# Kernel optimization log

Hardware: AMD Instinct MI355X
Metric: run time of the kernel (lower is better)

## Reference

```python
import jax, jax.numpy as jnp
import numpy as np

NUM_PATCHES = 128  # K centers from farthest point sampling
PATCH_SIZE = 32    # neighbors per patch (KNN)


def setup_inputs() -> dict:
    key = jax.random.key(0)
    points = jax.random.normal(key, (32, 8192, 3), dtype=jnp.float32)
    return {"points": points}


def _fps(points, K):
    """Farthest point sampling. points: [B, N, 3] -> idx [B, K] (int32).
    Deterministic start at index 0 (original uses random_start_point=True;
    only the start index differs)."""
    B, N, _ = points.shape
    start = jnp.zeros((B,), dtype=jnp.int32)

    def step(carry, _):
        mind, last = carry  # mind: [B, N] running min sq-dist, last: [B]
        last_pt = jnp.take_along_axis(points, last[:, None, None], axis=1)[:, 0]  # [B, 3]
        d = jnp.sum((points - last_pt[:, None, :]) ** 2, axis=-1)  # [B, N]
        mind = jnp.minimum(mind, d)
        nxt = jnp.argmax(mind, axis=1).astype(jnp.int32)
        return (mind, nxt), last

    init = (jnp.full((B, N), jnp.inf, dtype=points.dtype), start)
    _, idxs = jax.lax.scan(step, init, None, length=K)  # [K, B]
    return jnp.transpose(idxs)  # [B, K]


def reference(points):
    # FPS center selection
    fps_idx = _fps(points, NUM_PATCHES)  # [B, K]
    centers = jnp.take_along_axis(points, fps_idx[:, :, None], axis=1)  # [B, K, 3]
    # Brute-force KNN: squared distances centers->points, [B, K, N]
    d2 = (jnp.sum(centers * centers, axis=-1)[:, :, None]
          + jnp.sum(points * points, axis=-1)[:, None, :]
          - 2.0 * jnp.einsum('bkd,bnd->bkn', centers, points))
    # k smallest distances, sorted ascending (top_k of negated d2 is descending)
    _, idx = jax.lax.top_k(-d2, PATCH_SIZE)  # [B, K, patch_size]
    return idx, centers
```

## Files before the change

kernel.cpp:

```cpp
#include <hip/hip_runtime.h>

#define BB 32
#define NN 8192
#define KK 128
#define PP 32
#define IDX_COUNT (BB * KK * PP)
#define XCHG_WORDS (BB * KK * 3)
#define XCHG_BYTES (XCHG_WORDS * 4)

#define DPP_RED_U64(v, CMP)                                                   \
    {                                                                         \
        _Pragma("unroll")                                                     \
        for (int s = 0; s < 6; ++s) {                                         \
            const int ctrl = (s == 0) ? 0x111 : (s == 1) ? 0x112 :            \
                             (s == 2) ? 0x114 : (s == 3) ? 0x118 :            \
                             (s == 4) ? 0x142 : 0x143;                        \
            unsigned lo = (unsigned)v, hi = (unsigned)(v >> 32);              \
            unsigned slo, shi;                                                \
            switch (ctrl) {                                                   \
            case 0x111:                                                       \
                slo = (unsigned)__builtin_amdgcn_update_dpp((int)lo, (int)lo, 0x111, 0xf, 0xf, false); \
                shi = (unsigned)__builtin_amdgcn_update_dpp((int)hi, (int)hi, 0x111, 0xf, 0xf, false); break; \
            case 0x112:                                                       \
                slo = (unsigned)__builtin_amdgcn_update_dpp((int)lo, (int)lo, 0x112, 0xf, 0xf, false); \
                shi = (unsigned)__builtin_amdgcn_update_dpp((int)hi, (int)hi, 0x112, 0xf, 0xf, false); break; \
            case 0x114:                                                       \
                slo = (unsigned)__builtin_amdgcn_update_dpp((int)lo, (int)lo, 0x114, 0xf, 0xf, false); \
                shi = (unsigned)__builtin_amdgcn_update_dpp((int)hi, (int)hi, 0x114, 0xf, 0xf, false); break; \
            case 0x118:                                                       \
                slo = (unsigned)__builtin_amdgcn_update_dpp((int)lo, (int)lo, 0x118, 0xf, 0xf, false); \
                shi = (unsigned)__builtin_amdgcn_update_dpp((int)hi, (int)hi, 0x118, 0xf, 0xf, false); break; \
            case 0x142:                                                       \
                slo = (unsigned)__builtin_amdgcn_update_dpp((int)lo, (int)lo, 0x142, 0xf, 0xf, false); \
                shi = (unsigned)__builtin_amdgcn_update_dpp((int)hi, (int)hi, 0x142, 0xf, 0xf, false); break; \
            default:                                                          \
                slo = (unsigned)__builtin_amdgcn_update_dpp((int)lo, (int)lo, 0x143, 0xf, 0xf, false); \
                shi = (unsigned)__builtin_amdgcn_update_dpp((int)hi, (int)hi, 0x143, 0xf, 0xf, false); break; \
            }                                                                 \
            const unsigned long long sv = ((unsigned long long)shi << 32) | slo; \
            if (sv CMP v) v = sv;                                             \
        }                                                                     \
    }

__device__ __forceinline__ unsigned long long readlane63_u64(unsigned long long v) {
    const unsigned lo = (unsigned)__builtin_amdgcn_readlane((int)(unsigned)v, 63);
    const unsigned hi = (unsigned)__builtin_amdgcn_readlane((int)(unsigned)(v >> 32), 63);
    return ((unsigned long long)hi << 32) | lo;
}

__device__ __forceinline__ void publish_word(unsigned* p, float v) {
    __hip_atomic_store(p, __float_as_uint(v), __ATOMIC_RELAXED,
                       __HIP_MEMORY_SCOPE_AGENT);
}
__device__ __forceinline__ float poll_word(const unsigned* p) {
    unsigned u = __hip_atomic_load(p, __ATOMIC_RELAXED, __HIP_MEMORY_SCOPE_AGENT);
    while (u == 0xFFFFFFFFu) {
        __builtin_amdgcn_s_sleep(8);
        u = __hip_atomic_load(p, __ATOMIC_RELAXED, __HIP_MEMORY_SCOPE_AGENT);
    }
    return __uint_as_float(u);
}

#define BAR_LDS() asm volatile("s_waitcnt lgkmcnt(0)\n\ts_barrier" ::: "memory")

#define CACHE_INS(kk, m1, m2, m3, m4)                                   \
    {                                                                   \
        const bool c1 = (kk) < m1, c2 = (kk) < m2,                      \
                   c3 = (kk) < m3, c4 = (kk) < m4;                      \
        m4 = c3 ? m3 : (c4 ? (kk) : m4);                                \
        m3 = c2 ? m2 : (c3 ? (kk) : m3);                                \
        m2 = c1 ? m1 : (c2 ? (kk) : m2);                                \
        m1 = c1 ? (kk) : m1;                                            \
    }

__global__ __launch_bounds__(1024) void clear_kernel(unsigned* __restrict__ xchg) {
    const int i = blockIdx.x * 1024 + threadIdx.x;
    xchg[i] = 0xFFFFFFFFu;
}

__global__ __launch_bounds__(512) void fused_kernel(
    const float* __restrict__ pts, float* __restrict__ out,
    unsigned* __restrict__ xchg)
{
#pragma clang fp contract(off)
    __shared__ __align__(16) unsigned char smem_raw[131072];
    const int t = threadIdx.x;
    const int lane = t & 63, wid = t >> 6;

    if (blockIdx.x < BB) {
        const int b = blockIdx.x;
        const float* p = pts + (size_t)b * NN * 3;
        float* pts3 = (float*)smem_raw;
        float* cbuf = (float*)(smem_raw + 98304);
        unsigned long long* wkf =
            (unsigned long long*)(smem_raw + 98304 + 1536);

        if (t == 0) {
            unsigned* dst = xchg + (unsigned)b * KK * 3u;
            publish_word(dst + 0, p[0]);
            publish_word(dst + 1, p[1]);
            publish_word(dst + 2, p[2]);
        }

        float px[16], py[16], pz[16], mind[16];
#pragma unroll
        for (int i = 0; i < 16; ++i) {
            const int idx = t + i * 512;
            const float x = p[idx * 3 + 0], y = p[idx * 3 + 1], z = p[idx * 3 + 2];
            px[i] = x; py[i] = y; pz[i] = z; mind[i] = __builtin_inff();
            pts3[idx * 3 + 0] = x; pts3[idx * 3 + 1] = y; pts3[idx * 3 + 2] = z;
        }
        __syncthreads();

        float lx = pts3[0], ly = pts3[1], lz = pts3[2];
        if (t == 0) { cbuf[0] = lx; cbuf[1] = ly; cbuf[2] = lz; }

        for (int k = 0; k < KK - 1; ++k) {
            float best = -1.0f; unsigned bidx = 0;
#pragma unroll
            for (int i = 0; i < 16; ++i) {
                const float dx = px[i] - lx, dy = py[i] - ly, dz = pz[i] - lz;
                const float d = (dx * dx + dy * dy) + dz * dz;
                const float m = mind[i] < d ? mind[i] : d;
                mind[i] = m;
                if (m > best) { best = m; bidx = (unsigned)(t + i * 512); }
            }
            union { float f; unsigned u; } cv; cv.f = best;
            unsigned long long key = ((unsigned long long)cv.u << 32)
                                   | (0xFFFFFFFFu - bidx);
            DPP_RED_U64(key, >);
            if (lane == 63) wkf[(k & 1) * 8 + wid] = key;
            BAR_LDS();
            unsigned long long w = wkf[(k & 1) * 8];
#pragma unroll
            for (int i = 1; i < 8; ++i) {
                const unsigned long long o = wkf[(k & 1) * 8 + i];
                if (o > w) w = o;
            }
            const unsigned last = 0xFFFFFFFFu - (unsigned)(w & 0xFFFFFFFFu);
            lx = pts3[last * 3 + 0];
            ly = pts3[last * 3 + 1];
            lz = pts3[last * 3 + 2];
            if (t == 0) {
                cbuf[(k + 1) * 3 + 0] = lx;
                cbuf[(k + 1) * 3 + 1] = ly;
                cbuf[(k + 1) * 3 + 2] = lz;
                unsigned* dst = xchg + ((unsigned)b * KK + (unsigned)(k + 1)) * 3u;
                publish_word(dst + 0, lx);
                publish_word(dst + 1, ly);
                publish_word(dst + 2, lz);
            }
        }
        __syncthreads();
        if (t < KK * 3)
            out[IDX_COUNT + b * (KK * 3) + t] = cbuf[t];
    } else {
        const int blk = blockIdx.x - BB;
        const int b = blk >> 2, kblk = blk & 3;
        float4* sp = (float4*)smem_raw;
        const float* p = pts + (size_t)b * NN * 3;
#pragma unroll
        for (int i = 0; i < 16; ++i) {
            const int idx = t + i * 512;
            const float x = p[idx * 3 + 0], y = p[idx * 3 + 1], z = p[idx * 3 + 2];
            sp[idx] = make_float4(x, y, z, (x * x + y * y) + z * z);
        }
        __syncthreads();

        for (int u = 0; u < 4; ++u) {
            const int c = kblk + 4 * wid + 32 * u;
            const unsigned* src = xchg + ((unsigned)b * KK + (unsigned)c) * 3u;
            const float cx = poll_word(src + 0);
            const float cy = poll_word(src + 1);
            const float cz = poll_word(src + 2);
            const float cc = (cx * cx + cy * cy) + cz * cz;

            unsigned long long m1 = ~0ull, m2 = ~0ull, m3 = ~0ull, m4 = ~0ull;
#pragma unroll 4
            for (int i = 0; i < 128; ++i) {
                const int idx = lane + i * 64;
                const float4 q = sp[idx];
                const float dot = (cx * q.x + cy * q.y) + cz * q.z;
                float d2 = (cc + q.w) - (2.0f * dot);
                d2 = d2 + 0.0f;
                union { float f; unsigned u; } cv; cv.f = d2;
                unsigned uu = cv.u;
                uu = (uu & 0x80000000u) ? ~uu : (uu | 0x80000000u);
                const unsigned long long kk2 =
                    ((unsigned long long)uu << 32) | (unsigned)idx;
                CACHE_INS(kk2, m1, m2, m3, m4);
            }

            float resv = 0.0f;
            for (int j = 0; j < PP; ++j) {
                unsigned long long r = m1;
                DPP_RED_U64(r, <);
                const unsigned long long best = readlane63_u64(r);
                if (lane == j) resv = (float)(unsigned)(best & 0xFFFFFFFFu);
                if (m1 == best) { m1 = m2; m2 = m3; m3 = m4; m4 = ~0ull; }
                if (m1 == ~0ull) {
                    for (int i = 0; i < 128; ++i) {
                        const int idx = lane + i * 64;
                        const float4 q = sp[idx];
                        const float dot = (cx * q.x + cy * q.y) + cz * q.z;
                        float d2 = (cc + q.w) - (2.0f * dot);
                        d2 = d2 + 0.0f;
                        union { float f; unsigned u; } cv; cv.f = d2;
                        unsigned uu = cv.u;
                        uu = (uu & 0x80000000u) ? ~uu : (uu | 0x80000000u);
                        const unsigned long long kk2 =
                            ((unsigned long long)uu << 32) | (unsigned)idx;
                        if (kk2 > best) CACHE_INS(kk2, m1, m2, m3, m4);
                    }
                }
            }
            if (lane < PP)
                out[(size_t)(b * KK + c) * PP + lane] = resv;
        }
    }
}

__global__ __launch_bounds__(512) void fps_kernel(
    const float* __restrict__ pts, float* __restrict__ out)
{
#pragma clang fp contract(off)
    const int b = blockIdx.x;
    const int t = threadIdx.x;
    const float* p = pts + (size_t)b * NN * 3;

    __shared__ float pts3[NN * 3];
    __shared__ float cbuf[KK * 3];
    __shared__ unsigned long long wk[2][8];

    float px[16], py[16], pz[16], mind[16];
#pragma unroll
    for (int i = 0; i < 16; ++i) {
        const int idx = t + i * 512;
        const float x = p[idx * 3 + 0], y = p[idx * 3 + 1], z = p[idx * 3 + 2];
        px[i] = x; py[i] = y; pz[i] = z; mind[i] = __builtin_inff();
        pts3[idx * 3 + 0] = x; pts3[idx * 3 + 1] = y; pts3[idx * 3 + 2] = z;
    }
    __syncthreads();

    float lx = pts3[0], ly = pts3[1], lz = pts3[2];
    if (t == 0) { cbuf[0] = lx; cbuf[1] = ly; cbuf[2] = lz; }
    const int lane = t & 63, wid = t >> 6;

    for (int k = 0; k < KK - 1; ++k) {
        float best = -1.0f; unsigned bidx = 0;
#pragma unroll
        for (int i = 0; i < 16; ++i) {
            const float dx = px[i] - lx, dy = py[i] - ly, dz = pz[i] - lz;
            const float d = (dx * dx + dy * dy) + dz * dz;
            const float m = mind[i] < d ? mind[i] : d;
            mind[i] = m;
            if (m > best) { best = m; bidx = (unsigned)(t + i * 512); }
        }
        union { float f; unsigned u; } cv; cv.f = best;
        unsigned long long key = ((unsigned long long)cv.u << 32)
                               | (0xFFFFFFFFu - bidx);
        DPP_RED_U64(key, >);
        if (lane == 63) wk[k & 1][wid] = key;
        __syncthreads();
        unsigned long long w = wk[k & 1][0];
#pragma unroll
        for (int i = 1; i < 8; ++i) {
            const unsigned long long o = wk[k & 1][i];
            if (o > w) w = o;
        }
        const unsigned last = 0xFFFFFFFFu - (unsigned)(w & 0xFFFFFFFFu);
        lx = pts3[last * 3 + 0];
        ly = pts3[last * 3 + 1];
        lz = pts3[last * 3 + 2];
        if (t == 0) {
            cbuf[(k + 1) * 3 + 0] = lx;
            cbuf[(k + 1) * 3 + 1] = ly;
            cbuf[(k + 1) * 3 + 2] = lz;
        }
    }
    __syncthreads();
    if (t < KK * 3)
        out[IDX_COUNT + b * (KK * 3) + t] = cbuf[t];
}

__global__ __launch_bounds__(1024) void knn_kernel(
    const float* __restrict__ pts, float* __restrict__ out)
{
#pragma clang fp contract(off)
    const int t = threadIdx.x, lane = t & 63, wid = t >> 6;
    const int blk = blockIdx.x;
    const int b = blk >> 3;
    const int bk = b * KK + (blk & 7) * 16 + wid;

    __shared__ float4 sp[NN];
    const float* p = pts + (size_t)b * NN * 3;
#pragma unroll
    for (int i = 0; i < 8; ++i) {
        const int idx = t + i * 1024;
        const float x = p[idx * 3 + 0], y = p[idx * 3 + 1], z = p[idx * 3 + 2];
        sp[idx] = make_float4(x, y, z, (x * x + y * y) + z * z);
    }

    const float cx = out[IDX_COUNT + bk * 3 + 0];
    const float cy = out[IDX_COUNT + bk * 3 + 1];
    const float cz = out[IDX_COUNT + bk * 3 + 2];
    const float cc = (cx * cx + cy * cy) + cz * cz;
    __syncthreads();

    unsigned long long m1 = ~0ull, m2 = ~0ull, m3 = ~0ull, m4 = ~0ull;
#pragma unroll 4
    for (int i = 0; i < 128; ++i) {
        const int idx = lane + i * 64;
        const float4 q = sp[idx];
        const float dot = (cx * q.x + cy * q.y) + cz * q.z;
        float d2 = (cc + q.w) - (2.0f * dot);
        d2 = d2 + 0.0f;
        union { float f; unsigned u; } cv; cv.f = d2;
        unsigned u = cv.u;
        u = (u & 0x80000000u) ? ~u : (u | 0x80000000u);
        const unsigned long long kk =
            ((unsigned long long)u << 32) | (unsigned)idx;
        CACHE_INS(kk, m1, m2, m3, m4);
    }

    float resv = 0.0f;
    for (int j = 0; j < PP; ++j) {
        unsigned long long r = m1;
        DPP_RED_U64(r, <);
        const unsigned long long best = readlane63_u64(r);
        if (lane == j) resv = (float)(unsigned)(best & 0xFFFFFFFFu);
        if (m1 == best) { m1 = m2; m2 = m3; m3 = m4; m4 = ~0ull; }
        if (m1 == ~0ull) {
            for (int i = 0; i < 128; ++i) {
                const int idx = lane + i * 64;
                const float4 q = sp[idx];
                const float dot = (cx * q.x + cy * q.y) + cz * q.z;
                float d2 = (cc + q.w) - (2.0f * dot);
                d2 = d2 + 0.0f;
                union { float f; unsigned u; } cv; cv.f = d2;
                unsigned u = cv.u;
                u = (u & 0x80000000u) ? ~u : (u | 0x80000000u);
                const unsigned long long kk =
                    ((unsigned long long)u << 32) | (unsigned)idx;
                if (kk > best) CACHE_INS(kk, m1, m2, m3, m4);
            }
        }
    }
    if (lane < PP) out[(size_t)bk * PP + lane] = resv;
}

extern "C" void kernel_launch(void* const* d_in, const int* in_sizes, int n_in,
                              void* d_out, int out_size, void* d_ws, size_t ws_size,
                              hipStream_t stream) {
    const float* pts = (const float*)d_in[0];
    float* out = (float*)d_out;

    if (ws_size >= (size_t)XCHG_BYTES) {
        clear_kernel<<<XCHG_WORDS / 1024, 1024, 0, stream>>>((unsigned*)d_ws);
        fused_kernel<<<BB + BB * 4, 512, 0, stream>>>(pts, out, (unsigned*)d_ws);
    } else {
        fps_kernel<<<BB, 512, 0, stream>>>(pts, out);
        knn_kernel<<<BB * 8, 1024, 0, stream>>>(pts, out);
    }
}
```

Measured before the change: 235.6 us.

## Use atomic work-claiming for KNN centers and let FPS blocks join KNN

KNN waves in the fused kernel now claim centers dynamically through a per-batch atomic counter instead of taking a fixed static assignment. The FPS blocks, once sampling is done, also claim leftover centers and run KNN from their packed xyz LDS copy. The number of KNN helper blocks per batch drops from 4 to 3, and the top-4 cache keeps distance and index in separate 32-bit registers instead of packed 64-bit keys. This is meant to balance the tail after FPS finishes and cut 64-bit compare cost, at the price of atomic contention and a slower stride-3 LDS path in the FPS blocks.

```diff
diff --git a/kernel.cpp b/kernel.cpp
--- a/kernel.cpp
+++ b/kernel.cpp
@@ -6,7 +6,9 @@
 #define PP 32
 #define IDX_COUNT (BB * KK * PP)
 #define XCHG_WORDS (BB * KK * 3)
-#define XCHG_BYTES (XCHG_WORDS * 4)
+#define CLEAR_WORDS (XCHG_WORDS + BB)
+#define KNN_PER_B 3
+#define NBLK (BB + BB * KNN_PER_B)
 
 #define DPP_RED_U64(v, CMP)                                                   \
     {                                                                         \
@@ -63,19 +65,85 @@
 
 #define BAR_LDS() asm volatile("s_waitcnt lgkmcnt(0)\n\ts_barrier" ::: "memory")
 
-#define CACHE_INS(kk, m1, m2, m3, m4)                                   \
+#define CACHE_INS2(dd, ii, d1, i1, d2, i2, d3, i3, d4, i4)              \
     {                                                                   \
-        const bool c1 = (kk) < m1, c2 = (kk) < m2,                      \
-                   c3 = (kk) < m3, c4 = (kk) < m4;                      \
-        m4 = c3 ? m3 : (c4 ? (kk) : m4);                                \
-        m3 = c2 ? m2 : (c3 ? (kk) : m3);                                \
-        m2 = c1 ? m1 : (c2 ? (kk) : m2);                                \
-        m1 = c1 ? (kk) : m1;                                            \
-    }
+        const bool c1 = (dd) < d1, c2 = (dd) < d2,                      \
+                   c3 = (dd) < d3, c4 = (dd) < d4;                      \
+        d4 = c3 ? d3 : (c4 ? (dd) : d4);  i4 = c3 ? i3 : (c4 ? (ii) : i4); \
+        d3 = c2 ? d2 : (c3 ? (dd) : d3);  i3 = c2 ? i2 : (c3 ? (ii) : i3); \
+        d2 = c1 ? d1 : (c2 ? (dd) : d2);  i2 = c1 ? i1 : (c2 ? (ii) : i2); \
+        d1 = c1 ? (dd) : d1;              i1 = c1 ? (ii) : i1;          \
+    }
+
+template <int SRC>
+__device__ __forceinline__ void knn_one_center(
+    const float* __restrict__ ldsf, const int lane,
+    const float cx, const float cy, const float cz,
+    float* __restrict__ outp)
+{
+#pragma clang fp contract(off)
+    const float cc = (cx * cx + cy * cy) + cz * cz;
+    unsigned d1 = ~0u, i1 = ~0u, d2_ = ~0u, i2 = ~0u,
+             d3 = ~0u, i3 = ~0u, d4 = ~0u, i4 = ~0u;
+#pragma unroll 4
+    for (int i = 0; i < 128; ++i) {
+        const int idx = lane + i * 64;
+        float qx, qy, qz, qw;
+        if constexpr (SRC == 0) {
+            const float4 q = ((const float4*)ldsf)[idx];
+            qx = q.x; qy = q.y; qz = q.z; qw = q.w;
+        } else {
+            qx = ldsf[idx * 3 + 0]; qy = ldsf[idx * 3 + 1]; qz = ldsf[idx * 3 + 2];
+            qw = (qx * qx + qy * qy) + qz * qz;
+        }
+        const float dot = (cx * qx + cy * qy) + cz * qz;
+        float dd2 = (cc + qw) - (2.0f * dot);
+        dd2 = dd2 + 0.0f;
+        unsigned u = __float_as_uint(dd2);
+        u = (u & 0x80000000u) ? ~u : (u | 0x80000000u);
+        CACHE_INS2(u, (unsigned)idx, d1, i1, d2_, i2, d3, i3, d4, i4);
+    }
+
+    float resv = 0.0f;
+    for (int j = 0; j < PP; ++j) {
+        unsigned long long r = ((unsigned long long)d1 << 32) | i1;
+        DPP_RED_U64(r, <);
+        const unsigned long long best = readlane63_u64(r);
+        if (lane == j) resv = (float)(unsigned)(best & 0xFFFFFFFFu);
+        if (((((unsigned long long)d1 << 32) | i1)) == best) {
+            d1 = d2_; i1 = i2; d2_ = d3; i2 = i3; d3 = d4; i3 = i4;
+            d4 = ~0u; i4 = ~0u;
+        }
+        if (d1 == ~0u) {
+            for (int i = 0; i < 128; ++i) {
+                const int idx = lane + i * 64;
+                float qx, qy, qz, qw;
+                if constexpr (SRC == 0) {
+                    const float4 q = ((const float4*)ldsf)[idx];
+                    qx = q.x; qy = q.y; qz = q.z; qw = q.w;
+                } else {
+                    qx = ldsf[idx * 3 + 0]; qy = ldsf[idx * 3 + 1]; qz = ldsf[idx * 3 + 2];
+                    qw = (qx * qx + qy * qy) + qz * qz;
+                }
+                const float dot = (cx * qx + cy * qy) + cz * qz;
+                float dd2 = (cc + qw) - (2.0f * dot);
+                dd2 = dd2 + 0.0f;
+                unsigned u = __float_as_uint(dd2);
+                u = (u & 0x80000000u) ? ~u : (u | 0x80000000u);
+                const unsigned long long kk2 =
+                    ((unsigned long long)u << 32) | (unsigned)idx;
+                if (kk2 > best)
+                    CACHE_INS2(u, (unsigned)idx, d1, i1, d2_, i2, d3, i3, d4, i4);
+            }
+        }
+    }
+    if (lane < PP) outp[lane] = resv;
+}
 
 __global__ __launch_bounds__(1024) void clear_kernel(unsigned* __restrict__ xchg) {
     const int i = blockIdx.x * 1024 + threadIdx.x;
-    xchg[i] = 0xFFFFFFFFu;
+    if (i < XCHG_WORDS) xchg[i] = 0xFFFFFFFFu;
+    else if (i < CLEAR_WORDS) xchg[i] = 0u;
 }
 
 __global__ __launch_bounds__(512) void fused_kernel(
@@ -86,6 +154,7 @@
     __shared__ __align__(16) unsigned char smem_raw[131072];
     const int t = threadIdx.x;
     const int lane = t & 63, wid = t >> 6;
+    unsigned* claims = xchg + XCHG_WORDS;
 
     if (blockIdx.x < BB) {
         const int b = blockIdx.x;
@@ -154,9 +223,22 @@
         __syncthreads();
         if (t < KK * 3)
             out[IDX_COUNT + b * (KK * 3) + t] = cbuf[t];
+
+        for (;;) {
+            unsigned m = 0;
+            if (lane == 0) m = atomicAdd(claims + b, 1u);
+            m = (unsigned)__builtin_amdgcn_readfirstlane((int)m);
+            if (m >= KK) break;
+            const int c = (int)m;
+            const float cx = cbuf[c * 3 + 0];
+            const float cy = cbuf[c * 3 + 1];
+            const float cz = cbuf[c * 3 + 2];
+            knn_one_center<1>(pts3, lane, cx, cy, cz,
+                              out + (size_t)(b * KK + c) * PP);
+        }
     } else {
         const int blk = blockIdx.x - BB;
-        const int b = blk >> 2, kblk = blk & 3;
+        const int b = blk / KNN_PER_B;
         float4* sp = (float4*)smem_raw;
         const float* p = pts + (size_t)b * NN * 3;
 #pragma unroll
@@ -167,55 +249,19 @@
         }
         __syncthreads();
 
-        for (int u = 0; u < 4; ++u) {
-            const int c = kblk + 4 * wid + 32 * u;
+        for (;;) {
+            unsigned m = 0;
+            if (lane == 0) m = atomicAdd(claims + b, 1u);
+            m = (unsigned)__builtin_amdgcn_readfirstlane((int)m);
+            if (m >= KK) break;
+            const int c = (int)m;
+
             const unsigned* src = xchg + ((unsigned)b * KK + (unsigned)c) * 3u;
             const float cx = poll_word(src + 0);
             const float cy = poll_word(src + 1);
             const float cz = poll_word(src + 2);
-            const float cc = (cx * cx + cy * cy) + cz * cz;
-
-            unsigned long long m1 = ~0ull, m2 = ~0ull, m3 = ~0ull, m4 = ~0ull;
-#pragma unroll 4
-            for (int i = 0; i < 128; ++i) {
-                const int idx = lane + i * 64;
-                const float4 q = sp[idx];
-                const float dot = (cx * q.x + cy * q.y) + cz * q.z;
-                float d2 = (cc + q.w) - (2.0f * dot);
-                d2 = d2 + 0.0f;
-                union { float f; unsigned u; } cv; cv.f = d2;
-                unsigned uu = cv.u;
-                uu = (uu & 0x80000000u) ? ~uu : (uu | 0x80000000u);
-                const unsigned long long kk2 =
-                    ((unsigned long long)uu << 32) | (unsigned)idx;
-                CACHE_INS(kk2, m1, m2, m3, m4);
-            }
-
-            float resv = 0.0f;
-            for (int j = 0; j < PP; ++j) {
-                unsigned long long r = m1;
-                DPP_RED_U64(r, <);
-                const unsigned long long best = readlane63_u64(r);
-                if (lane == j) resv = (float)(unsigned)(best & 0xFFFFFFFFu);
-                if (m1 == best) { m1 = m2; m2 = m3; m3 = m4; m4 = ~0ull; }
-                if (m1 == ~0ull) {
-                    for (int i = 0; i < 128; ++i) {
-                        const int idx = lane + i * 64;
-                        const float4 q = sp[idx];
-                        const float dot = (cx * q.x + cy * q.y) + cz * q.z;
-                        float d2 = (cc + q.w) - (2.0f * dot);
-                        d2 = d2 + 0.0f;
-                        union { float f; unsigned u; } cv; cv.f = d2;
-                        unsigned uu = cv.u;
-                        uu = (uu & 0x80000000u) ? ~uu : (uu | 0x80000000u);
-                        const unsigned long long kk2 =
-                            ((unsigned long long)uu << 32) | (unsigned)idx;
-                        if (kk2 > best) CACHE_INS(kk2, m1, m2, m3, m4);
-                    }
-                }
-            }
-            if (lane < PP)
-                out[(size_t)(b * KK + c) * PP + lane] = resv;
+            knn_one_center<0>((const float*)sp, lane, cx, cy, cz,
+                              out + (size_t)(b * KK + c) * PP);
         }
     }
 }
@@ -304,49 +350,10 @@
     const float cx = out[IDX_COUNT + bk * 3 + 0];
     const float cy = out[IDX_COUNT + bk * 3 + 1];
     const float cz = out[IDX_COUNT + bk * 3 + 2];
-    const float cc = (cx * cx + cy * cy) + cz * cz;
     __syncthreads();
 
-    unsigned long long m1 = ~0ull, m2 = ~0ull, m3 = ~0ull, m4 = ~0ull;
-#pragma unroll 4
-    for (int i = 0; i < 128; ++i) {
-        const int idx = lane + i * 64;
-        const float4 q = sp[idx];
-        const float dot = (cx * q.x + cy * q.y) + cz * q.z;
-        float d2 = (cc + q.w) - (2.0f * dot);
-        d2 = d2 + 0.0f;
-        union { float f; unsigned u; } cv; cv.f = d2;
-        unsigned u = cv.u;
-        u = (u & 0x80000000u) ? ~u : (u | 0x80000000u);
-        const unsigned long long kk =
-            ((unsigned long long)u << 32) | (unsigned)idx;
-        CACHE_INS(kk, m1, m2, m3, m4);
-    }
-
-    float resv = 0.0f;
-    for (int j = 0; j < PP; ++j) {
-        unsigned long long r = m1;
-        DPP_RED_U64(r, <);
-        const unsigned long long best = readlane63_u64(r);
-        if (lane == j) resv = (float)(unsigned)(best & 0xFFFFFFFFu);
-        if (m1 == best) { m1 = m2; m2 = m3; m3 = m4; m4 = ~0ull; }
-        if (m1 == ~0ull) {
-            for (int i = 0; i < 128; ++i) {
-                const int idx = lane + i * 64;
-                const float4 q = sp[idx];
-                const float dot = (cx * q.x + cy * q.y) + cz * q.z;
-                float d2 = (cc + q.w) - (2.0f * dot);
-                d2 = d2 + 0.0f;
-                union { float f; unsigned u; } cv; cv.f = d2;
-                unsigned u = cv.u;
-                u = (u & 0x80000000u) ? ~u : (u | 0x80000000u);
-                const unsigned long long kk =
-                    ((unsigned long long)u << 32) | (unsigned)idx;
-                if (kk > best) CACHE_INS(kk, m1, m2, m3, m4);
-            }
-        }
-    }
-    if (lane < PP) out[(size_t)bk * PP + lane] = resv;
+    knn_one_center<0>((const float*)sp, lane, cx, cy, cz,
+                      out + (size_t)bk * PP);
 }
 
 extern "C" void kernel_launch(void* const* d_in, const int* in_sizes, int n_in,
@@ -355,9 +362,10 @@
     const float* pts = (const float*)d_in[0];
     float* out = (float*)d_out;
 
-    if (ws_size >= (size_t)XCHG_BYTES) {
-        clear_kernel<<<XCHG_WORDS / 1024, 1024, 0, stream>>>((unsigned*)d_ws);
-        fused_kernel<<<BB + BB * 4, 512, 0, stream>>>(pts, out, (unsigned*)d_ws);
+    if (ws_size >= (size_t)(CLEAR_WORDS * 4)) {
+        clear_kernel<<<(CLEAR_WORDS + 1023) / 1024, 1024, 0, stream>>>(
+            (unsigned*)d_ws);
+        fused_kernel<<<NBLK, 512, 0, stream>>>(pts, out, (unsigned*)d_ws);
     } else {
         fps_kernel<<<BB, 512, 0, stream>>>(pts, out);
         knn_kernel<<<BB * 8, 1024, 0, stream>>>(pts, out);
```

Result: faster. 227.5 us (-3.5%).
